# Optimization experiments

Measured on AMD Instinct MI355X. Metric: run time of the kernel, lower is better.

The kernel has to match this reference:

```python
import jax, jax.numpy as jnp
import numpy as np

B, T, D = 1, 2048, 3072
N, K, H = 16, 8, 256  # heads, kv heads, head dim
SOFT_CAP = 50.0
WINDOW = 1024
ROPE_BASE = 10000.0
ROPE_SCALE = 1.0
K_MASK = -2.3819763e+38
EPS = 1e-6


def rms_norm(x, scale=None):
    var = jnp.mean(jnp.square(x), axis=-1, keepdims=True)
    y = x * jax.lax.rsqrt(var + EPS)
    if scale is not None:
        y = y * (1.0 + scale)
    return y


def apply_rope(x, positions):
    # x: [B, T, n, H], positions: [B, T] int
    half = x.shape[-1] // 2
    fraction = 2.0 * jnp.arange(half, dtype=jnp.float32) / x.shape[-1]
    timescale = ROPE_BASE ** fraction  # [half]
    sinusoid = positions[..., None].astype(jnp.float32) / timescale  # [B,T,half]
    sinusoid = sinusoid[..., None, :] / ROPE_SCALE  # [B,T,1,half]
    sin, cos = jnp.sin(sinusoid), jnp.cos(sinusoid)
    first, second = jnp.split(x, 2, axis=-1)
    out = jnp.concatenate([first * cos - second * sin,
                           second * cos + first * sin], axis=-1)
    return out.astype(x.dtype)


def setup_inputs() -> dict:
    key = jax.random.key(0)
    ks = jax.random.split(key, 6)
    x = jax.random.normal(ks[0], (B, T, D), jnp.float32)
    segment_pos = jnp.broadcast_to(jnp.arange(T, dtype=jnp.int32), (B, T))
    attn_mask = jnp.broadcast_to(jnp.tril(jnp.ones((T, T), bool)), (B, T, T))
    w_q = jax.random.normal(ks[1], (N, D, H), jnp.float32) * 0.02
    w_kv = jax.random.normal(ks[2], (2, K, D, H), jnp.float32) * 0.02
    w_out = jax.random.normal(ks[3], (N, H, D), jnp.float32) * 0.02
    q_scale = jax.random.normal(ks[4], (H,), jnp.float32) * 0.1
    k_scale = jax.random.normal(ks[5], (H,), jnp.float32) * 0.1
    return {"x": x, "segment_pos": segment_pos, "attn_mask": attn_mask,
            "w_q": w_q, "w_kv": w_kv, "w_out": w_out,
            "q_scale": q_scale, "k_scale": k_scale}


def reference(x, segment_pos, attn_mask, w_q, w_kv, w_out, q_scale, k_scale):
    # Q projection + QK-RMSNorm + RoPE
    q = jnp.einsum('BTD,NDH->BTNH', x, w_q)
    q = rms_norm(q, q_scale)
    q = apply_rope(q, segment_pos)
    # fused KV projection
    kv = jnp.einsum('BSD,CKDH->CBSKH', x, w_kv)
    k_proj, v_proj = kv[0], kv[1]
    k_proj = rms_norm(k_proj, k_scale)
    v_proj = rms_norm(v_proj)  # value norm has no scale
    k_proj = apply_rope(k_proj, segment_pos)
    # GQA logits: q [B,T,K,G,H] x k [B,S,K,H]
    G = N // K
    qg = q.reshape(B, T, K, G, H)
    logits = jnp.einsum('BTKGH,BSKH->BTKGS', qg, k_proj).reshape(B, T, N, T)
    # logit soft-capping
    logits = jnp.tanh(logits / SOFT_CAP) * SOFT_CAP
    # sliding-window mask (cache_positions == segment_pos since cache is None)
    pos_q = segment_pos[:, :, None]
    pos_k = segment_pos[:, None, :]
    sliding = (pos_k > pos_q - WINDOW) & (pos_k < pos_q + WINDOW)  # [B,T,S]
    mask = attn_mask & sliding
    padded = jnp.where(mask[:, :, None, :], logits, K_MASK)
    probs = jax.nn.softmax(padded, axis=-1).astype(k_proj.dtype)
    enc = jnp.einsum('BTKGS,BSKH->BTKGH',
                     probs.reshape(B, T, K, G, T), v_proj).reshape(B, T, N, H)
    attn_output = jnp.einsum('BTNH,NHD->BTD', enc, w_out)
    return attn_output
```

## Files before the change

kernel.cpp:

```cpp
#include <hip/hip_runtime.h>
#include <math.h>

#define T_SEQ 2048
#define D_MODEL 3072
#define NQ 16
#define NKV 8
#define HD 256
#define NHEADS_TOT 32
#define QKV_COLS 8192
#define SOFT_CAP 50.0f
#define WINDOW 1024
#define K_MASK -2.3819763e38f

typedef __attribute__((ext_vector_type(8))) short bf16x8;
typedef __attribute__((ext_vector_type(4))) float f32x4;

__device__ __forceinline__ unsigned short f2bf(float f) {
    union { float f; unsigned u; } v; v.f = f;
    unsigned r = (v.u + 0x7fff + ((v.u >> 16) & 1)) >> 16;
    return (unsigned short)r;
}
__device__ __forceinline__ float bf2f(unsigned short u) {
    union { unsigned u; float f; } v; v.u = ((unsigned)u) << 16;
    return v.f;
}

__device__ __forceinline__ void gl_lds16(const unsigned short* g, unsigned short* l) {
    __builtin_amdgcn_global_load_lds(
        (const __attribute__((address_space(1))) void*)g,
        (__attribute__((address_space(3))) void*)l, 16, 0, 0);
}

__global__ __launch_bounds__(256) void k_convert(const float* __restrict__ src,
                                                 unsigned short* __restrict__ dst, int n4) {
    int i = blockIdx.x * 256 + threadIdx.x;
    if (i >= n4) return;
    float4 v = ((const float4*)src)[i];
    ushort4 o;
    o.x = f2bf(v.x); o.y = f2bf(v.y); o.z = f2bf(v.z); o.w = f2bf(v.w);
    ((ushort4*)dst)[i] = o;
}

__global__ __launch_bounds__(256) void k_transpose_bf16(const float* __restrict__ src,
                                                        unsigned short* __restrict__ dst,
                                                        int R, int C) {
    __shared__ float tile[32][33];
    int b = blockIdx.z;
    src += (size_t)b * R * C;
    dst += (size_t)b * R * C;
    int c0 = blockIdx.x * 32, r0 = blockIdx.y * 32;
    int tx = threadIdx.x, ty = threadIdx.y;
    #pragma unroll
    for (int i = ty; i < 32; i += 8)
        tile[i][tx] = src[(size_t)(r0 + i) * C + c0 + tx];
    __syncthreads();
    #pragma unroll
    for (int i = ty; i < 32; i += 8)
        dst[(size_t)(c0 + i) * R + r0 + tx] = f2bf(tile[tx][i]);
}

__global__ __launch_bounds__(256) void k_transpose_v(const unsigned short* __restrict__ src,
                                                     unsigned short* __restrict__ dst) {
    __shared__ unsigned short tile[32][34];
    int kk = blockIdx.z;
    src += (size_t)kk * T_SEQ * HD;
    dst += (size_t)kk * HD * T_SEQ;
    int h0 = blockIdx.x * 32, t0 = blockIdx.y * 32;
    int tx = threadIdx.x, ty = threadIdx.y;
    #pragma unroll
    for (int i = ty; i < 32; i += 8)
        tile[i][tx] = src[(size_t)(t0 + i) * HD + h0 + tx];
    __syncthreads();
    #pragma unroll
    for (int i = ty; i < 32; i += 8)
        dst[(size_t)(h0 + i) * T_SEQ + t0 + tx] = tile[tx][i];
}

__global__ __launch_bounds__(128) void k_trig(const int* __restrict__ spos,
                                              float2* __restrict__ tbl) {
    int t = blockIdx.x, hh = threadIdx.x;
    float fr = (float)hh * (1.0f / 128.0f);
    float ts = __expf(fr * 9.210340371976184f);
    float ang = (float)spos[t] / ts;
    float2 sc;
    sc.x = __sinf(ang);
    sc.y = __cosf(ang);
    tbl[(size_t)t * 128 + hh] = sc;
}

__global__ __launch_bounds__(256, 2) void k_gemm1(const unsigned short* __restrict__ A,
                                                  const unsigned short* __restrict__ BT,
                                                  unsigned short* __restrict__ C,
                                                  int M, int N, int Kd) {
    __shared__ unsigned short As[128 * 64];
    __shared__ unsigned short Bs[256 * 64];
    const int tid = threadIdx.x;
    const int wave = tid >> 6, lane = tid & 63;
    const int col = lane & 15, quad = lane >> 4;
    const int wr = wave & 1, wc = wave >> 1;

    int p = blockIdx.x;
    int xcd = p & 7, q = p >> 3;
    int i_t = q & 15, jj = q >> 4;
    const int m0 = i_t * 128, n0 = (jj * 8 + xcd) * 256;

    const int lrow = lane >> 3, lchk = lane & 7;
    int soffA[4], soffB[8];
    #pragma unroll
    for (int s = 0; s < 4; s++) {
        int r = wave * 32 + s * 8 + lrow;
        soffA[s] = r * Kd + ((lchk ^ (r & 7)) * 8);
    }
    #pragma unroll
    for (int s = 0; s < 8; s++) {
        int r = wave * 64 + s * 8 + lrow;
        soffB[s] = r * Kd + ((lchk ^ (r & 7)) * 8);
    }
    const unsigned short* Ab = A + (size_t)m0 * Kd;
    const unsigned short* Bb = BT + (size_t)n0 * Kd;

    f32x4 acc[4][8];
    #pragma unroll
    for (int i = 0; i < 4; i++)
        #pragma unroll
        for (int j = 0; j < 8; j++)
            acc[i][j] = (f32x4){0.f, 0.f, 0.f, 0.f};

    const int sw = col & 7;

    for (int k0 = 0; k0 < Kd; k0 += 64) {
        #pragma unroll
        for (int s = 0; s < 4; s++)
            gl_lds16(Ab + soffA[s] + k0, &As[(wave * 32 + s * 8) * 64]);
        #pragma unroll
        for (int s = 0; s < 8; s++)
            gl_lds16(Bb + soffB[s] + k0, &Bs[(wave * 64 + s * 8) * 64]);
        __syncthreads();

        #pragma unroll
        for (int kk = 0; kk < 2; kk++) {
            const int chko = ((kk * 4 + quad) ^ sw) * 8;
            bf16x8 af[4];
            #pragma unroll
            for (int i = 0; i < 4; i++)
                af[i] = *(const bf16x8*)&As[(wr * 64 + i * 16 + col) * 64 + chko];
            #pragma unroll
            for (int j = 0; j < 8; j++) {
                bf16x8 bfr = *(const bf16x8*)&Bs[(wc * 128 + j * 16 + col) * 64 + chko];
                #pragma unroll
                for (int i = 0; i < 4; i++)
                    acc[i][j] = __builtin_amdgcn_mfma_f32_16x16x32_bf16(af[i], bfr, acc[i][j], 0, 0, 0);
            }
        }
        __syncthreads();
    }

    #pragma unroll
    for (int i = 0; i < 4; i++) {
        int row = m0 + wr * 64 + i * 16 + quad * 4;
        #pragma unroll
        for (int j = 0; j < 8; j++) {
            int c = n0 + wc * 128 + j * 16 + col;
            #pragma unroll
            for (int r = 0; r < 4; r++)
                C[(size_t)(row + r) * N + c] = f2bf(acc[i][j][r]);
        }
    }
}

__global__ __launch_bounds__(256) void k_gemm2(const unsigned short* __restrict__ A,
                                               const unsigned short* __restrict__ BT,
                                               float* __restrict__ C,
                                               int M, int N, int Kd) {
    __shared__ unsigned short As[128 * 128];
    __shared__ unsigned short Bs[64 * 128];
    const int tid = threadIdx.x;
    const int wave = tid >> 6, lane = tid & 63;
    const int col = lane & 15, quad = lane >> 4;

    int p = blockIdx.x;
    int xcd = p & 7, q = p >> 3;
    int i_t = q % 16, jj = q / 16;
    const int m0 = i_t * 128, n0 = (jj * 8 + xcd) * 64;

    const int lrow = lane >> 4, lchk = lane & 15;
    int soffA[8], soffB[4];
    #pragma unroll
    for (int s = 0; s < 8; s++) {
        int r = wave * 32 + s * 4 + lrow;
        soffA[s] = r * Kd + ((lchk ^ (r & 7)) * 8);
    }
    #pragma unroll
    for (int s = 0; s < 4; s++) {
        int r = wave * 16 + s * 4 + lrow;
        soffB[s] = r * Kd + ((lchk ^ (r & 7)) * 8);
    }
    const unsigned short* Ab = A + (size_t)m0 * Kd;
    const unsigned short* Bb = BT + (size_t)n0 * Kd;

    f32x4 acc[2][4];
    #pragma unroll
    for (int i = 0; i < 2; i++)
        #pragma unroll
        for (int j = 0; j < 4; j++)
            acc[i][j] = (f32x4){0.f, 0.f, 0.f, 0.f};

    const int sw = col & 7;

    for (int k0 = 0; k0 < Kd; k0 += 128) {
        #pragma unroll
        for (int s = 0; s < 8; s++)
            gl_lds16(Ab + soffA[s] + k0, &As[(wave * 32 + s * 4) * 128]);
        #pragma unroll
        for (int s = 0; s < 4; s++)
            gl_lds16(Bb + soffB[s] + k0, &Bs[(wave * 16 + s * 4) * 128]);
        __syncthreads();

        #pragma unroll
        for (int kk = 0; kk < 4; kk++) {
            const int chko = ((kk * 4 + quad) ^ sw) * 8;
            bf16x8 af[2], bfr[4];
            #pragma unroll
            for (int i = 0; i < 2; i++)
                af[i] = *(const bf16x8*)&As[(wave * 32 + i * 16 + col) * 128 + chko];
            #pragma unroll
            for (int j = 0; j < 4; j++)
                bfr[j] = *(const bf16x8*)&Bs[(j * 16 + col) * 128 + chko];
            #pragma unroll
            for (int i = 0; i < 2; i++)
                #pragma unroll
                for (int j = 0; j < 4; j++)
                    acc[i][j] = __builtin_amdgcn_mfma_f32_16x16x32_bf16(af[i], bfr[j], acc[i][j], 0, 0, 0);
        }
        __syncthreads();
    }

    #pragma unroll
    for (int i = 0; i < 2; i++) {
        int row = m0 + wave * 32 + i * 16 + quad * 4;
        #pragma unroll
        for (int j = 0; j < 4; j++) {
            int c = n0 + j * 16 + col;
            #pragma unroll
            for (int r = 0; r < 4; r++)
                C[(size_t)(row + r) * N + c] = acc[i][j][r];
        }
    }
}

__global__ __launch_bounds__(256) void k_norm_rope(const unsigned short* __restrict__ qkv,
                                                   const float2* __restrict__ trig,
                                                   const float* __restrict__ qscale,
                                                   const float* __restrict__ kscale,
                                                   unsigned short* __restrict__ qh,
                                                   unsigned short* __restrict__ kh,
                                                   unsigned short* __restrict__ vh) {
    const int t = blockIdx.x, y = blockIdx.y, h = threadIdx.x;
    __shared__ float wsum[4][4];
    __shared__ float ybuf[3][256];

    float val[4];
    #pragma unroll
    for (int g = 0; g < 4; g++)
        val[g] = bf2f(qkv[(size_t)t * QKV_COLS + (y + g * 8) * HD + h]);

    float ssg[4];
    #pragma unroll
    for (int g = 0; g < 4; g++) {
        float ss = val[g] * val[g];
        #pragma unroll
        for (int m = 1; m < 64; m <<= 1) ss += __shfl_xor(ss, m, 64);
        ssg[g] = ss;
    }
    if ((h & 63) == 0) {
        #pragma unroll
        for (int g = 0; g < 4; g++) wsum[g][h >> 6] = ssg[g];
    }
    __syncthreads();

    float2 sc = trig[(size_t)t * 128 + (h & 127)];
    float qs = 1.0f + qscale[h], ks = 1.0f + kscale[h];

    float yv[4];
    #pragma unroll
    for (int g = 0; g < 4; g++) {
        float tot = wsum[g][0] + wsum[g][1] + wsum[g][2] + wsum[g][3];
        float yy = val[g] * rsqrtf(tot * (1.0f / 256.0f) + 1e-6f);
        if (g < 2) yy *= qs;
        else if (g == 2) yy *= ks;
        yv[g] = yy;
        if (g < 3) ybuf[g][h] = yy;
    }
    __syncthreads();

    #pragma unroll
    for (int g = 0; g < 3; g++) {
        float other = ybuf[g][(h < 128) ? (h + 128) : (h - 128)];
        float outv = (h < 128) ? (yv[g] * sc.y - other * sc.x)
                               : (yv[g] * sc.y + other * sc.x);
        int slot = y + g * 8;
        if (slot < 16)
            qh[((size_t)slot * T_SEQ + t) * HD + h] = f2bf(outv);
        else
            kh[((size_t)(slot - 16) * T_SEQ + t) * HD + h] = f2bf(outv);
    }
    vh[((size_t)y * T_SEQ + t) * HD + h] = f2bf(yv[3]);
}

__global__ __launch_bounds__(256) void k_attn(const unsigned short* __restrict__ qh,
                                              const unsigned short* __restrict__ kh,
                                              const unsigned short* __restrict__ vT,
                                              unsigned short* __restrict__ enc) {
    __shared__ unsigned short Ks[32 * 256];
    __shared__ unsigned short Vs[256 * 32];
    __shared__ unsigned short Pl[4][16 * 40];

    const int tid = threadIdx.x;
    const int wave = tid >> 6, lane = tid & 63;
    const int col = lane & 15, quad = lane >> 4;
    const int kk = blockIdx.x;
    const int t0b = blockIdx.y * 32;
    const int headSel = wave & 1, rowSel = wave >> 1;
    const int n = kk * 2 + headSel;
    const int tw = t0b + rowSel * 16;

    const unsigned short* qp = qh + ((size_t)n * T_SEQ + tw) * HD;
    const unsigned short* kp = kh + (size_t)kk * T_SEQ * HD;
    const unsigned short* vp = vT + (size_t)kk * HD * T_SEQ;

    bf16x8 qf[8];
    #pragma unroll
    for (int c = 0; c < 8; c++)
        qf[c] = *(const bf16x8*)(qp + (size_t)col * HD + c * 32 + quad * 8);

    int preK[4], preV[4], ldsKo[4], ldsVo[4];
    #pragma unroll
    for (int i = 0; i < 4; i++) {
        int krow = 2 * (wave * 4 + i) + (lane >> 5);
        int kpos = lane & 31;
        preK[i] = krow * HD + ((kpos ^ (krow & 7)) * 8);
        ldsKo[i] = (wave * 4 + i) * 512;
        int vh2 = (wave * 4 + i) * 16 + (lane >> 2);
        int vpp = lane & 3;
        preV[i] = vh2 * T_SEQ + ((vpp ^ (vh2 & 3)) * 8);
        ldsVo[i] = (wave * 4 + i) * 512;
    }

    f32x4 o[16];
    #pragma unroll
    for (int h = 0; h < 16; h++) o[h] = (f32x4){0.f, 0.f, 0.f, 0.f};
    float lsum[4] = {0.f, 0.f, 0.f, 0.f};

    int s_begin = t0b - (WINDOW - 1);
    if (s_begin < 0) s_begin = 0;
    s_begin &= ~31;
    const int s_end = t0b + 32;

    for (int s0 = s_begin; s0 < s_end; s0 += 32) {
        #pragma unroll
        for (int i = 0; i < 4; i++)
            gl_lds16(kp + (size_t)s0 * HD + preK[i], &Ks[ldsKo[i]]);
        #pragma unroll
        for (int i = 0; i < 4; i++)
            gl_lds16(vp + (size_t)s0 + preV[i], &Vs[ldsVo[i]]);
        __syncthreads();

        f32x4 S0 = (f32x4){0.f, 0.f, 0.f, 0.f};
        f32x4 S1 = (f32x4){0.f, 0.f, 0.f, 0.f};
        #pragma unroll
        for (int c = 0; c < 8; c++) {
            bf16x8 kf = *(const bf16x8*)&Ks[(size_t)col * HD + (((c * 4 + quad) ^ (col & 7)) * 8)];
            S0 = __builtin_amdgcn_mfma_f32_16x16x32_bf16(qf[c], kf, S0, 0, 0, 0);
        }
        #pragma unroll
        for (int c = 0; c < 8; c++) {
            bf16x8 kf = *(const bf16x8*)&Ks[(size_t)(16 + col) * HD + (((c * 4 + quad) ^ (col & 7)) * 8)];
            S1 = __builtin_amdgcn_mfma_f32_16x16x32_bf16(qf[c], kf, S1, 0, 0, 0);
        }

        #pragma unroll
        for (int r = 0; r < 4; r++) {
            int t = tw + quad * 4 + r;
            int sA = s0 + col, sB = sA + 16;
            bool vA = (sA <= t) && (sA >= t - (WINDOW - 1));
            bool vB = (sB <= t) && (sB >= t - (WINDOW - 1));
            float eA = __expf(S0[r] * (2.0f / SOFT_CAP));
            float eB = __expf(S1[r] * (2.0f / SOFT_CAP));
            float rA = __builtin_amdgcn_rcpf(eA + 1.0f);
            float rB = __builtin_amdgcn_rcpf(eB + 1.0f);
            float pA = __expf(SOFT_CAP - 2.0f * SOFT_CAP * rA);
            float pB = __expf(SOFT_CAP - 2.0f * SOFT_CAP * rB);
            pA = vA ? pA : 0.0f;
            pB = vB ? pB : 0.0f;
            lsum[r] += pA + pB;
            Pl[wave][(quad * 4 + r) * 40 + col] = f2bf(pA);
            Pl[wave][(quad * 4 + r) * 40 + 16 + col] = f2bf(pB);
        }

        bf16x8 pf = *(const bf16x8*)&Pl[wave][col * 40 + quad * 8];

        #pragma unroll
        for (int ht = 0; ht < 16; ht++) {
            int h = ht * 16 + col;
            bf16x8 vf = *(const bf16x8*)&Vs[(size_t)h * 32 + ((quad ^ (h & 3)) * 8)];
            o[ht] = __builtin_amdgcn_mfma_f32_16x16x32_bf16(pf, vf, o[ht], 0, 0, 0);
        }
        __syncthreads();
    }

    #pragma unroll
    for (int r = 0; r < 4; r++) {
        #pragma unroll
        for (int m = 1; m < 16; m <<= 1)
            lsum[r] += __shfl_xor(lsum[r], m, 16);
        lsum[r] = 1.0f / lsum[r];
    }
    #pragma unroll
    for (int ht = 0; ht < 16; ht++) {
        #pragma unroll
        for (int r = 0; r < 4; r++) {
            int t = tw + quad * 4 + r;
            enc[(size_t)t * (NQ * HD) + n * HD + ht * 16 + col] = f2bf(o[ht][r] * lsum[r]);
        }
    }
}

extern "C" void kernel_launch(void* const* d_in, const int* in_sizes, int n_in,
                              void* d_out, int out_size, void* d_ws, size_t ws_size,
                              hipStream_t stream) {
    const float* x       = (const float*)d_in[0];
    const int*   spos    = (const int*)d_in[1];
    const float* w_q     = (const float*)d_in[3];
    const float* w_kv    = (const float*)d_in[4];
    const float* w_out   = (const float*)d_in[5];
    const float* q_scale = (const float*)d_in[6];
    const float* k_scale = (const float*)d_in[7];
    float* out = (float*)d_out;

    char* ws = (char*)d_ws;
    unsigned short* xb     = (unsigned short*)(ws + 0);
    unsigned short* vh     = (unsigned short*)(ws + 0);
    float2*         trig   = (float2*)(ws + 8388608);
    unsigned short* wT     = (unsigned short*)(ws + 12582912);
    unsigned short* wToutb = (unsigned short*)(ws + 12582912);
    unsigned short* encb   = (unsigned short*)(ws + 37748736);
    unsigned short* qkv    = (unsigned short*)(ws + 62914560);
    unsigned short* qh     = (unsigned short*)(ws + 96468992);
    unsigned short* kh     = (unsigned short*)(ws + 113246208);
    unsigned short* vT     = (unsigned short*)(ws + 121634816);

    k_convert<<<dim3((T_SEQ * D_MODEL / 4 + 255) / 256), dim3(256), 0, stream>>>(
        x, xb, T_SEQ * D_MODEL / 4);
    k_transpose_bf16<<<dim3(HD / 32, D_MODEL / 32, NQ), dim3(32, 8), 0, stream>>>(
        w_q, wT, D_MODEL, HD);
    k_transpose_bf16<<<dim3(HD / 32, D_MODEL / 32, 16), dim3(32, 8), 0, stream>>>(
        w_kv, wT + (size_t)4096 * D_MODEL, D_MODEL, HD);
    k_gemm1<<<dim3((T_SEQ / 128) * (QKV_COLS / 256)), dim3(256), 0, stream>>>(
        xb, wT, qkv, T_SEQ, QKV_COLS, D_MODEL);
    k_trig<<<dim3(T_SEQ), dim3(128), 0, stream>>>(spos, trig);
    k_transpose_bf16<<<dim3(D_MODEL / 32, 4096 / 32, 1), dim3(32, 8), 0, stream>>>(
        w_out, wToutb, 4096, D_MODEL);
    k_norm_rope<<<dim3(T_SEQ, 8), dim3(256), 0, stream>>>(
        qkv, trig, q_scale, k_scale, qh, kh, vh);
    k_transpose_v<<<dim3(HD / 32, T_SEQ / 32, NKV), dim3(32, 8), 0, stream>>>(vh, vT);
    k_attn<<<dim3(NKV, T_SEQ / 32), dim3(256), 0, stream>>>(qh, kh, vT, encb);
    k_gemm2<<<dim3((T_SEQ / 128) * (D_MODEL / 64)), dim3(256), 0, stream>>>(
        encb, wToutb, out, T_SEQ, D_MODEL, NQ * HD);
}
```

Measured before the change: 489.3 us.

## Rewrite QKV GEMM as 256x256 tile double-buffered pipeline with 8 waves

The QKV projection GEMM moves from a 128x256 tile with 4 waves and a single LDS buffer to a 256x256 tile with 8 waves and double-buffered LDS. Global-to-LDS loads for the next K step are interleaved with MFMA groups, using explicit vmcnt waits, barriers and setprio. This is meant to hide load latency behind compute and raise data reuse per tile. In exchange it uses 128KB of LDS and a hard-coded K-loop count, so the kernel assumes K=3072 and cannot run two blocks per CU.

```diff
diff --git a/kernel.cpp b/kernel.cpp
--- a/kernel.cpp
+++ b/kernel.cpp
@@ -88,82 +88,137 @@
     tbl[(size_t)t * 128 + hh] = sc;
 }
 
-__global__ __launch_bounds__(256, 2) void k_gemm1(const unsigned short* __restrict__ A,
+__global__ __launch_bounds__(512, 2) void k_gemm1(const unsigned short* __restrict__ A,
                                                   const unsigned short* __restrict__ BT,
                                                   unsigned short* __restrict__ C,
                                                   int M, int N, int Kd) {
-    __shared__ unsigned short As[128 * 64];
-    __shared__ unsigned short Bs[256 * 64];
+    __shared__ unsigned short As[2 * 256 * 64];
+    __shared__ unsigned short Bs[2 * 256 * 64];
+
     const int tid = threadIdx.x;
     const int wave = tid >> 6, lane = tid & 63;
     const int col = lane & 15, quad = lane >> 4;
-    const int wr = wave & 1, wc = wave >> 1;
+    const int wr = wave >> 2, wc = wave & 3;
 
     int p = blockIdx.x;
     int xcd = p & 7, q = p >> 3;
-    int i_t = q & 15, jj = q >> 4;
-    const int m0 = i_t * 128, n0 = (jj * 8 + xcd) * 256;
-
-    const int lrow = lane >> 3, lchk = lane & 7;
-    int soffA[4], soffB[8];
-    #pragma unroll
-    for (int s = 0; s < 4; s++) {
-        int r = wave * 32 + s * 8 + lrow;
-        soffA[s] = r * Kd + ((lchk ^ (r & 7)) * 8);
-    }
-    #pragma unroll
-    for (int s = 0; s < 8; s++) {
-        int r = wave * 64 + s * 8 + lrow;
-        soffB[s] = r * Kd + ((lchk ^ (r & 7)) * 8);
-    }
+    int i_t = q & 7, jj = q >> 3;
+    const int m0 = i_t * 256, n0 = (jj * 8 + xcd) * 256;
+
+    const int lr3 = lane >> 3, lc7 = lane & 7;
+    const int cxor = (lc7 ^ lr3) * 8;
+    const int rbA = (wave >> 2) * 128 + (wave & 3) * 16;
+    const int rbB = (wave >> 1) * 64 + (wave & 1) * 16;
+
     const unsigned short* Ab = A + (size_t)m0 * Kd;
     const unsigned short* Bb = BT + (size_t)n0 * Kd;
 
-    f32x4 acc[4][8];
-    #pragma unroll
-    for (int i = 0; i < 4; i++)
-        #pragma unroll
-        for (int j = 0; j < 8; j++)
-            acc[i][j] = (f32x4){0.f, 0.f, 0.f, 0.f};
-
+#define STG_A(bufp, mh, kt) do {                                                          \
+    int rb_ = rbA + (mh) * 64;                                                            \
+    gl_lds16(Ab + (size_t)(rb_ + lr3) * Kd + cxor + (kt) * 64, (bufp) + rb_ * 64);        \
+    gl_lds16(Ab + (size_t)(rb_ + 8 + lr3) * Kd + cxor + (kt) * 64, (bufp) + (rb_ + 8) * 64); \
+  } while (0)
+#define STG_B(bufp, nh, kt) do {                                                          \
+    int rb_ = rbB + (nh) * 32;                                                            \
+    gl_lds16(Bb + (size_t)(rb_ + lr3) * Kd + cxor + (kt) * 64, (bufp) + rb_ * 64);        \
+    gl_lds16(Bb + (size_t)(rb_ + 8 + lr3) * Kd + cxor + (kt) * 64, (bufp) + (rb_ + 8) * 64); \
+  } while (0)
+
+    f32x4 acc[8][4];
+    #pragma unroll
+    for (int i = 0; i < 8; i++)
+        #pragma unroll
+        for (int j2 = 0; j2 < 4; j2++)
+            acc[i][j2] = (f32x4){0.f, 0.f, 0.f, 0.f};
+
+    bf16x8 af[4][2];
+    bf16x8 bf0[2][2], bf1[2][2];
     const int sw = col & 7;
 
-    for (int k0 = 0; k0 < Kd; k0 += 64) {
-        #pragma unroll
-        for (int s = 0; s < 4; s++)
-            gl_lds16(Ab + soffA[s] + k0, &As[(wave * 32 + s * 8) * 64]);
-        #pragma unroll
-        for (int s = 0; s < 8; s++)
-            gl_lds16(Bb + soffB[s] + k0, &Bs[(wave * 64 + s * 8) * 64]);
-        __syncthreads();
-
-        #pragma unroll
-        for (int kk = 0; kk < 2; kk++) {
-            const int chko = ((kk * 4 + quad) ^ sw) * 8;
-            bf16x8 af[4];
-            #pragma unroll
-            for (int i = 0; i < 4; i++)
-                af[i] = *(const bf16x8*)&As[(wr * 64 + i * 16 + col) * 64 + chko];
-            #pragma unroll
-            for (int j = 0; j < 8; j++) {
-                bf16x8 bfr = *(const bf16x8*)&Bs[(wc * 128 + j * 16 + col) * 64 + chko];
-                #pragma unroll
-                for (int i = 0; i < 4; i++)
-                    acc[i][j] = __builtin_amdgcn_mfma_f32_16x16x32_bf16(af[i], bfr, acc[i][j], 0, 0, 0);
-            }
-        }
-        __syncthreads();
-    }
-
-    #pragma unroll
-    for (int i = 0; i < 4; i++) {
-        int row = m0 + wr * 64 + i * 16 + quad * 4;
-        #pragma unroll
-        for (int j = 0; j < 8; j++) {
-            int c = n0 + wc * 128 + j * 16 + col;
+#define LD_AF(bufp, mh) do {                                                              \
+    _Pragma("unroll") for (int i = 0; i < 4; i++) {                                       \
+      const unsigned short* rp_ = (bufp) + (wr * 128 + ((mh) * 4 + i) * 16 + col) * 64;   \
+      af[i][0] = *(const bf16x8*)(rp_ + (quad ^ sw) * 8);                                 \
+      af[i][1] = *(const bf16x8*)(rp_ + ((4 + quad) ^ sw) * 8);                           \
+    } } while (0)
+#define LD_BF(dst, bufp, nh) do {                                                         \
+    _Pragma("unroll") for (int j2 = 0; j2 < 2; j2++) {                                    \
+      const unsigned short* rp_ = (bufp) + (wc * 64 + ((nh) * 2 + j2) * 16 + col) * 64;   \
+      dst[j2][0] = *(const bf16x8*)(rp_ + (quad ^ sw) * 8);                               \
+      dst[j2][1] = *(const bf16x8*)(rp_ + ((4 + quad) ^ sw) * 8);                         \
+    } } while (0)
+#define MFMA16(mh, nh, BF) do {                                                           \
+    __builtin_amdgcn_s_setprio(1);                                                        \
+    _Pragma("unroll") for (int i = 0; i < 4; i++)                                         \
+      _Pragma("unroll") for (int j2 = 0; j2 < 2; j2++) {                                  \
+        acc[(mh)*4+i][(nh)*2+j2] = __builtin_amdgcn_mfma_f32_16x16x32_bf16(               \
+            af[i][0], BF[j2][0], acc[(mh)*4+i][(nh)*2+j2], 0, 0, 0);                      \
+        acc[(mh)*4+i][(nh)*2+j2] = __builtin_amdgcn_mfma_f32_16x16x32_bf16(               \
+            af[i][1], BF[j2][1], acc[(mh)*4+i][(nh)*2+j2], 0, 0, 0);                      \
+      }                                                                                   \
+    __builtin_amdgcn_s_setprio(0);                                                        \
+  } while (0)
+
+#define GROUP(CURA, CURB, NXTA, NXTB, S1, S2, ENDV, J) do {                               \
+                                                         \
+    LD_AF(CURA, 0); LD_BF(bf0, CURB, 0);                                                  \
+    if (S1) STG_A(NXTA, 1, (J) + 1);                                                      \
+    __builtin_amdgcn_s_barrier();                                                         \
+    MFMA16(0, 0, bf0);                                                                    \
+    __builtin_amdgcn_s_barrier();                                                         \
+                                              \
+    LD_BF(bf1, CURB, 1);                                                                  \
+    if (S1) STG_B(NXTB, 1, (J) + 1);                                                      \
+    __builtin_amdgcn_s_barrier();                                                         \
+    MFMA16(0, 1, bf1);                                                                    \
+    __builtin_amdgcn_s_barrier();                                                         \
+                                             \
+    LD_AF(CURA, 1);                                                                       \
+    if (S2) STG_A(CURA, 0, (J) + 2);                                                      \
+    __builtin_amdgcn_s_barrier();                                                         \
+    MFMA16(1, 0, bf0);                                                                    \
+    __builtin_amdgcn_s_barrier();                                                         \
+                                        \
+    if (S2) STG_B(CURB, 0, (J) + 2);                                                      \
+    __builtin_amdgcn_s_barrier();                                                         \
+    MFMA16(1, 1, bf1);                                                                    \
+    if ((ENDV) == 4)      asm volatile("s_waitcnt vmcnt(4)" ::: "memory");                \
+    else if ((ENDV) == 0) asm volatile("s_waitcnt vmcnt(0)" ::: "memory");                \
+    __builtin_amdgcn_s_barrier();                                                         \
+  } while (0)
+
+    unsigned short* A0 = As;          unsigned short* A1 = As + 16384;
+    unsigned short* B0 = Bs;          unsigned short* B1 = Bs + 16384;
+
+    STG_A(A0, 0, 0); STG_B(B0, 0, 0);
+    STG_A(A0, 1, 0); STG_B(B0, 1, 0);
+    STG_A(A1, 0, 1); STG_B(B1, 0, 1);
+    asm volatile("s_waitcnt vmcnt(4)" ::: "memory");
+    __builtin_amdgcn_s_barrier();
+
+    for (int kt = 0; kt < 46; kt += 2) {
+        GROUP(A0, B0, A1, B1, 1, 1, 4, kt);
+        GROUP(A1, B1, A0, B0, 1, 1, 4, kt + 1);
+    }
+    GROUP(A0, B0, A1, B1, 1, 0, 0, 46);
+    GROUP(A1, B1, A0, B0, 0, 0, -1, 47);
+
+#undef GROUP
+#undef MFMA16
+#undef LD_BF
+#undef LD_AF
+#undef STG_B
+#undef STG_A
+
+    #pragma unroll
+    for (int i = 0; i < 8; i++) {
+        int row = m0 + wr * 128 + i * 16 + quad * 4;
+        #pragma unroll
+        for (int j2 = 0; j2 < 4; j2++) {
+            int c = n0 + wc * 64 + j2 * 16 + col;
             #pragma unroll
             for (int r = 0; r < 4; r++)
-                C[(size_t)(row + r) * N + c] = f2bf(acc[i][j][r]);
+                C[(size_t)(row + r) * N + c] = f2bf(acc[i][j2][r]);
         }
     }
 }
@@ -455,7 +510,7 @@
         w_q, wT, D_MODEL, HD);
     k_transpose_bf16<<<dim3(HD / 32, D_MODEL / 32, 16), dim3(32, 8), 0, stream>>>(
         w_kv, wT + (size_t)4096 * D_MODEL, D_MODEL, HD);
-    k_gemm1<<<dim3((T_SEQ / 128) * (QKV_COLS / 256)), dim3(256), 0, stream>>>(
+    k_gemm1<<<dim3((T_SEQ / 256) * (QKV_COLS / 256)), dim3(512), 0, stream>>>(
         xb, wT, qkv, T_SEQ, QKV_COLS, D_MODEL);
     k_trig<<<dim3(T_SEQ), dim3(128), 0, stream>>>(spos, trig);
     k_transpose_bf16<<<dim3(D_MODEL / 32, 4096 / 32, 1), dim3(32, 8), 0, stream>>>(
```

Result: no change. 483.9 us (-1.1%).

## Double-buffer K/V tiles in attention and vectorize weight transpose kernels

Applied to the files above, without the earlier changes.

The attention kernel now keeps two LDS buffers for K and V and issues the global-to-LDS loads for the next 32-key tile before computing on the current one, so load latency can overlap the MFMA work. The fp32-to-bf16 weight transpose is rewritten to use 64x64 tiles with float4 reads and ushort4 writes, which cuts the number of memory transactions. The prefetch relies on a single barrier per iteration, and correctness depends on the async LDS writes landing before that barrier; LDS use per block roughly doubles, which may reduce occupancy.

```diff
diff --git a/kernel.cpp b/kernel.cpp
--- a/kernel.cpp
+++ b/kernel.cpp
@@ -44,19 +44,31 @@
 __global__ __launch_bounds__(256) void k_transpose_bf16(const float* __restrict__ src,
                                                         unsigned short* __restrict__ dst,
                                                         int R, int C) {
-    __shared__ float tile[32][33];
+    __shared__ unsigned short T[64][68];
     int b = blockIdx.z;
     src += (size_t)b * R * C;
     dst += (size_t)b * R * C;
-    int c0 = blockIdx.x * 32, r0 = blockIdx.y * 32;
-    int tx = threadIdx.x, ty = threadIdx.y;
-    #pragma unroll
-    for (int i = ty; i < 32; i += 8)
-        tile[i][tx] = src[(size_t)(r0 + i) * C + c0 + tx];
+    int c0 = blockIdx.x * 64, r0 = blockIdx.y * 64;
+    int tid = threadIdx.x;
+    int wv = tid >> 6, ln = tid & 63;
+    int rsub = (wv << 2) + (ln >> 4);
+    int cq = (ln & 15) << 2;
+    #pragma unroll
+    for (int p = 0; p < 4; p++) {
+        int row = p * 16 + rsub;
+        float4 v = *(const float4*)&src[(size_t)(r0 + row) * C + c0 + cq];
+        T[cq + 0][row] = f2bf(v.x);
+        T[cq + 1][row] = f2bf(v.y);
+        T[cq + 2][row] = f2bf(v.z);
+        T[cq + 3][row] = f2bf(v.w);
+    }
     __syncthreads();
     #pragma unroll
-    for (int i = ty; i < 32; i += 8)
-        dst[(size_t)(c0 + i) * R + r0 + tx] = f2bf(tile[tx][i]);
+    for (int q = 0; q < 4; q++) {
+        int crow = q * 16 + rsub;
+        ushort4 o = *(const ushort4*)&T[crow][cq];
+        *(ushort4*)&dst[(size_t)(c0 + crow) * R + r0 + cq] = o;
+    }
 }
 
 __global__ __launch_bounds__(256) void k_transpose_v(const unsigned short* __restrict__ src,
@@ -311,8 +323,8 @@
                                               const unsigned short* __restrict__ kh,
                                               const unsigned short* __restrict__ vT,
                                               unsigned short* __restrict__ enc) {
-    __shared__ unsigned short Ks[32 * 256];
-    __shared__ unsigned short Vs[256 * 32];
+    __shared__ unsigned short Ks[2][32 * 256];
+    __shared__ unsigned short Vs[2][256 * 32];
     __shared__ unsigned short Pl[4][16 * 40];
 
     const int tid = threadIdx.x;
@@ -356,25 +368,37 @@
     s_begin &= ~31;
     const int s_end = t0b + 32;
 
+    #pragma unroll
+    for (int i = 0; i < 4; i++)
+        gl_lds16(kp + (size_t)s_begin * HD + preK[i], &Ks[0][ldsKo[i]]);
+    #pragma unroll
+    for (int i = 0; i < 4; i++)
+        gl_lds16(vp + (size_t)s_begin + preV[i], &Vs[0][ldsVo[i]]);
+    __syncthreads();
+
+    int nb = 0;
     for (int s0 = s_begin; s0 < s_end; s0 += 32) {
-        #pragma unroll
-        for (int i = 0; i < 4; i++)
-            gl_lds16(kp + (size_t)s0 * HD + preK[i], &Ks[ldsKo[i]]);
-        #pragma unroll
-        for (int i = 0; i < 4; i++)
-            gl_lds16(vp + (size_t)s0 + preV[i], &Vs[ldsVo[i]]);
-        __syncthreads();
+        int s1 = s0 + 32;
+        if (s1 < s_end) {
+            #pragma unroll
+            for (int i = 0; i < 4; i++)
+                gl_lds16(kp + (size_t)s1 * HD + preK[i], &Ks[nb ^ 1][ldsKo[i]]);
+            #pragma unroll
+            for (int i = 0; i < 4; i++)
+                gl_lds16(vp + (size_t)s1 + preV[i], &Vs[nb ^ 1][ldsVo[i]]);
+        }
+        __builtin_amdgcn_sched_barrier(0);
 
         f32x4 S0 = (f32x4){0.f, 0.f, 0.f, 0.f};
         f32x4 S1 = (f32x4){0.f, 0.f, 0.f, 0.f};
         #pragma unroll
         for (int c = 0; c < 8; c++) {
-            bf16x8 kf = *(const bf16x8*)&Ks[(size_t)col * HD + (((c * 4 + quad) ^ (col & 7)) * 8)];
+            bf16x8 kf = *(const bf16x8*)&Ks[nb][(size_t)col * HD + (((c * 4 + quad) ^ (col & 7)) * 8)];
             S0 = __builtin_amdgcn_mfma_f32_16x16x32_bf16(qf[c], kf, S0, 0, 0, 0);
         }
         #pragma unroll
         for (int c = 0; c < 8; c++) {
-            bf16x8 kf = *(const bf16x8*)&Ks[(size_t)(16 + col) * HD + (((c * 4 + quad) ^ (col & 7)) * 8)];
+            bf16x8 kf = *(const bf16x8*)&Ks[nb][(size_t)(16 + col) * HD + (((c * 4 + quad) ^ (col & 7)) * 8)];
             S1 = __builtin_amdgcn_mfma_f32_16x16x32_bf16(qf[c], kf, S1, 0, 0, 0);
         }
 
@@ -402,10 +426,11 @@
         #pragma unroll
         for (int ht = 0; ht < 16; ht++) {
             int h = ht * 16 + col;
-            bf16x8 vf = *(const bf16x8*)&Vs[(size_t)h * 32 + ((quad ^ (h & 3)) * 8)];
+            bf16x8 vf = *(const bf16x8*)&Vs[nb][(size_t)h * 32 + ((quad ^ (h & 3)) * 8)];
             o[ht] = __builtin_amdgcn_mfma_f32_16x16x32_bf16(pf, vf, o[ht], 0, 0, 0);
         }
         __syncthreads();
+        nb ^= 1;
     }
 
     #pragma unroll
@@ -451,14 +476,14 @@
 
     k_convert<<<dim3((T_SEQ * D_MODEL / 4 + 255) / 256), dim3(256), 0, stream>>>(
         x, xb, T_SEQ * D_MODEL / 4);
-    k_transpose_bf16<<<dim3(HD / 32, D_MODEL / 32, NQ), dim3(32, 8), 0, stream>>>(
+    k_transpose_bf16<<<dim3(HD / 64, D_MODEL / 64, NQ), dim3(256), 0, stream>>>(
         w_q, wT, D_MODEL, HD);
-    k_transpose_bf16<<<dim3(HD / 32, D_MODEL / 32, 16), dim3(32, 8), 0, stream>>>(
+    k_transpose_bf16<<<dim3(HD / 64, D_MODEL / 64, 16), dim3(256), 0, stream>>>(
         w_kv, wT + (size_t)4096 * D_MODEL, D_MODEL, HD);
     k_gemm1<<<dim3((T_SEQ / 128) * (QKV_COLS / 256)), dim3(256), 0, stream>>>(
         xb, wT, qkv, T_SEQ, QKV_COLS, D_MODEL);
     k_trig<<<dim3(T_SEQ), dim3(128), 0, stream>>>(spos, trig);
-    k_transpose_bf16<<<dim3(D_MODEL / 32, 4096 / 32, 1), dim3(32, 8), 0, stream>>>(
+    k_transpose_bf16<<<dim3(D_MODEL / 64, 4096 / 64, 1), dim3(256), 0, stream>>>(
         w_out, wToutb, 4096, D_MODEL);
     k_norm_rope<<<dim3(T_SEQ, 8), dim3(256), 0, stream>>>(
         qkv, trig, q_scale, k_scale, qh, kh, vh);
```

After: 469.2 us. 1.04x faster.
